# Kernel optimization log

Hardware: AMD Instinct MI355X
Metric: run time of the kernel (lower is better)

The kernel has to match this reference:

```python
import jax, jax.numpy as jnp
import numpy as np

B, C, H, W = 4, 32, 256, 256


def _conv1x1(x, w, b):
    # 1x1 conv == channel-mixing matmul; x: [B,C,H,W], w: [Cout,Cin], b: [Cout]
    return jnp.einsum('oc,bchw->bohw', w, x) + b[None, :, None, None]


def setup_inputs() -> dict:
    key = jax.random.key(0)
    ks = jax.random.split(key, 12)
    inp = {
        'source': jax.random.normal(ks[0], (B, C, H, W), dtype=jnp.float32),
        'target': jax.random.normal(ks[1], (B, C, H, W), dtype=jnp.float32),
        # positional biases: torch.rand -> uniform [0,1)
        'P_v': jax.random.uniform(ks[2], (H, W), dtype=jnp.float32),
        'P_h': jax.random.uniform(ks[3], (W, H), dtype=jnp.float32),
        # 1x1 conv weights (Cout, Cin) + biases, kaiming-ish scale
        'w1v': jax.random.normal(ks[4], (C, C), dtype=jnp.float32) / np.sqrt(C),
        'b1v': jax.random.normal(ks[5], (C,), dtype=jnp.float32) * 0.01,
        'w2v': jax.random.normal(ks[6], (C, C), dtype=jnp.float32) / np.sqrt(C),
        'b2v': jax.random.normal(ks[7], (C,), dtype=jnp.float32) * 0.01,
        'w1h': jax.random.normal(ks[8], (C, C), dtype=jnp.float32) / np.sqrt(C),
        'b1h': jax.random.normal(ks[9], (C,), dtype=jnp.float32) * 0.01,
        'w2h': jax.random.normal(ks[10], (C, C), dtype=jnp.float32) / np.sqrt(C),
        'b2h': jax.random.normal(ks[11], (C,), dtype=jnp.float32) * 0.01,
    }
    return inp


def reference(source, target, P_v, P_h, w1v, b1v, w2v, b2v, w1h, b1h, w2h, b2h):
    # ---- vertical branch (attention along H, independent per column w) ----
    sv = _conv1x1(source + P_v, w1v, b1v)          # [B,C,H,W]
    tv = _conv1x1(target + P_v, w2v, b2v)          # [B,C,H,W]
    # scores_v[b,w,h,g] = sum_c sv[b,c,h,w] * tv[b,c,g,w]   (no softmax in original)
    scores_v = jnp.einsum('bchw,bcgw->bwhg', sv, tv)
    vertical = jnp.einsum('bwhg,bcgw->bchw', scores_v, target)

    # ---- horizontal branch (attention along W, independent per row h) ----
    # original adds P_h (w,h) to x.transpose(2,3); equivalent to adding P_h.T in BCHW
    sh = _conv1x1(source + P_h.T, w1h, b1h)        # [B,C,H,W]
    th = _conv1x1(target + P_h.T, w2h, b2h)        # [B,C,H,W]
    # scores_h[b,h,w,v] = sum_c sh[b,c,h,w] * th[b,c,h,v]
    scores_h = jnp.einsum('bchw,bchv->bhwv', sh, th)
    horizontal = jnp.einsum('bhwv,bchv->bchw', scores_h, target)

    return jnp.concatenate([horizontal, vertical], axis=1)  # [B,2C,H,W]
```

## Files before the change

### kernel.cpp

```cpp
#include <hip/hip_runtime.h>


#define OFF_GH   0
#define OFF_GV   1048576
#define OFF_QH   2097152
#define OFF_TSH  2129920
#define OFF_QV   2162688
#define OFF_TSV  2195456
#define OFF_PH   2228224
#define OFF_PV   2229504

#define FMA4(A, a4, b4) \
  A = fmaf((a4).x,(b4).x, fmaf((a4).y,(b4).y, fmaf((a4).z,(b4).z, fmaf((a4).w,(b4).w,(A)))))

__global__ __launch_bounds__(256) void prep_kernel(
    const float* __restrict__ w1, const float* __restrict__ b1,
    const float* __restrict__ w2, const float* __restrict__ b2,
    float* __restrict__ outp)
{
  __shared__ float lw1[1024], lw2[1024], lb1[32], lb2[32], lr1[32], lr2[32];
  const int t = threadIdx.x;
  for (int k = 0; k < 4; ++k) { lw1[t + 256*k] = w1[t + 256*k]; lw2[t + 256*k] = w2[t + 256*k]; }
  if (t < 32) { lb1[t] = b1[t]; lb2[t] = b2[t]; }
  __syncthreads();
  if (t < 32)      { float s = 0; for (int c = 0; c < 32; ++c) s += lw1[t*32 + c];      lr1[t] = s; }
  else if (t < 64) { int i = t - 32; float s = 0; for (int c = 0; c < 32; ++c) s += lw2[i*32 + c]; lr2[i] = s; }
  __syncthreads();
  for (int k = 0; k < 4; ++k) {
    const int e = t + 256*k, cp = e >> 5, cq = e & 31;
    float s = 0;
    for (int c1 = 0; c1 < 32; ++c1) s += lw1[c1*32 + cp] * lw2[c1*32 + cq];
    outp[e] = s;
  }
  if (t < 32)       { float s = 0; for (int c1 = 0; c1 < 32; ++c1) s += lw1[c1*32 + t]*lr2[c1];        outp[1024 + t] = s; }
  else if (t < 64)  { int i = t-32; float s = 0; for (int c1 = 0; c1 < 32; ++c1) s += lw1[c1*32+i]*lb2[c1]; outp[1056 + i] = s; }
  else if (t < 96)  { int i = t-64; float s = 0; for (int c1 = 0; c1 < 32; ++c1) s += lr1[c1]*lw2[c1*32+i]; outp[1088 + i] = s; }
  else if (t < 128) { int i = t-96; float s = 0; for (int c1 = 0; c1 < 32; ++c1) s += lb1[c1]*lw2[c1*32+i]; outp[1120 + i] = s; }
  else if (t == 128){ float s = 0; for (int i = 0; i < 32; ++i) s += lr1[i]*lr2[i]; outp[1152] = s; }
  else if (t == 129){ float s = 0; for (int i = 0; i < 32; ++i) s += lr1[i]*lb2[i]; outp[1153] = s; }
  else if (t == 130){ float s = 0; for (int i = 0; i < 32; ++i) s += lb1[i]*lr2[i]; outp[1154] = s; }
  else if (t == 131){ float s = 0; for (int i = 0; i < 32; ++i) s += lb1[i]*lb2[i]; outp[1155] = s; }
}

__global__ __launch_bounds__(256) void hgram_kernel(
    const float* __restrict__ T, const float* __restrict__ Ph,
    float* __restrict__ Gws, float* __restrict__ qws, float* __restrict__ tsws)
{
  __shared__ float tile[4][32*68];
  __shared__ float ptile[4][64];
  const int t = threadIdx.x, wave = t >> 6, lane = t & 63;
  const int x = blockIdx.x*4 + wave;
  const int b = x >> 8, r = x & 255;
  const int c1g = lane & 7, c2g = lane >> 3;
  const float* Trow = T + (b*32)*65536 + r*256;
  float* tw = tile[wave];
  float acc[4][4] = {};
  float qa[4] = {}, tsa[4] = {};
  const int l4 = lane >> 4, k16 = lane & 15;

  for (int ch = 0; ch < 4; ++ch) {
    const int k0 = ch*64;
    #pragma unroll
    for (int cc = 0; cc < 8; ++cc) {
      const int c = cc*4 + l4;
      const float4 v = *(const float4*)&Trow[c*65536 + k0 + k16*4];
      *(float4*)&tw[(l4*8 + cc)*68 + k16*4] = v;
    }
    ptile[wave][lane] = Ph[(k0 + lane)*256 + r];
    __syncthreads();
    #pragma unroll
    for (int g4 = 0; g4 < 16; ++g4) {
      float4 av[4], bv[4];
      const float4 p4 = *(const float4*)&ptile[wave][g4*4];
      #pragma unroll
      for (int i = 0; i < 4; ++i) av[i] = *(const float4*)&tw[(8*i + c1g)*68 + g4*4];
      #pragma unroll
      for (int j = 0; j < 4; ++j) bv[j] = *(const float4*)&tw[(8*j + c2g)*68 + g4*4];
      #pragma unroll
      for (int i = 0; i < 4; ++i)
        #pragma unroll
        for (int j = 0; j < 4; ++j) FMA4(acc[i][j], av[i], bv[j]);
      #pragma unroll
      for (int j = 0; j < 4; ++j) {
        FMA4(qa[j], p4, bv[j]);
        tsa[j] += (bv[j].x + bv[j].y) + (bv[j].z + bv[j].w);
      }
    }
    __syncthreads();
  }
  const int gb = x*1024;
  #pragma unroll
  for (int i = 0; i < 4; ++i) {
    float4 o; o.x = acc[i][0]; o.y = acc[i][1]; o.z = acc[i][2]; o.w = acc[i][3];
    *(float4*)&Gws[gb + (4*c1g + i)*32 + 4*c2g] = o;
  }
  if (c1g == 0) {
    float4 q4o; q4o.x = qa[0]; q4o.y = qa[1]; q4o.z = qa[2]; q4o.w = qa[3];
    float4 t4o; t4o.x = tsa[0]; t4o.y = tsa[1]; t4o.z = tsa[2]; t4o.w = tsa[3];
    *(float4*)&qws[x*32 + 4*c2g]  = q4o;
    *(float4*)&tsws[x*32 + 4*c2g] = t4o;
  }
}

__global__ __launch_bounds__(256) void vgram_kernel(
    const float* __restrict__ T, const float* __restrict__ Pv,
    float* __restrict__ Gws, float* __restrict__ qws, float* __restrict__ tsws)
{
  __shared__ float tile[32*292];
  __shared__ float ptile[4][2][36];
  const int blk = blockIdx.x;
  const int xcd = blk & 7, s = blk >> 3;
  const int b = s >> 2, w8l = s & 3;
  const int w0 = (xcd*4 + w8l)*8;
  const int t = threadIdx.x, wave = t >> 6, lane = t & 63;
  const int c1g = lane & 7, c2g = lane >> 3;
  const int lwb = wave*2;
  float acc[2][4][4] = {};
  float qa[2][4] = {}, tsa[2][4] = {};

  for (int chk = 0; chk < 8; ++chk) {
    const int g0 = chk*32;
    __syncthreads();
    #pragma unroll
    for (int p = 0; p < 8; ++p) {
      const int rowid = p*128 + (t >> 1);
      const int c = rowid >> 5, g = rowid & 31, j = t & 1;
      const float4 v = *(const float4*)&T[((b*32 + c)*256 + g0 + g)*256 + w0 + 4*j];
      float* d = &tile[((c&3)*8 + (c>>2))*292 + g];
      d[(4*j+0)*36] = v.x; d[(4*j+1)*36] = v.y; d[(4*j+2)*36] = v.z; d[(4*j+3)*36] = v.w;
    }
    if (lane < 32) ptile[wave][0][lane]    = Pv[(g0 + lane)*256      + w0 + lwb + 0];
    else           ptile[wave][1][lane-32] = Pv[(g0 + lane - 32)*256 + w0 + lwb + 1];
    __syncthreads();
    #pragma unroll
    for (int g4 = 0; g4 < 8; ++g4) {
      #pragma unroll
      for (int lw = 0; lw < 2; ++lw) {
        const int wo = (lwb + lw)*36 + g4*4;
        float4 av[4], bv[4];
        #pragma unroll
        for (int i = 0; i < 4; ++i) av[i] = *(const float4*)&tile[(8*i + c1g)*292 + wo];
        #pragma unroll
        for (int j = 0; j < 4; ++j) bv[j] = *(const float4*)&tile[(8*j + c2g)*292 + wo];
        const float4 p4 = *(const float4*)&ptile[wave][lw][g4*4];
        #pragma unroll
        for (int i = 0; i < 4; ++i)
          #pragma unroll
          for (int j = 0; j < 4; ++j) FMA4(acc[lw][i][j], av[i], bv[j]);
        #pragma unroll
        for (int j = 0; j < 4; ++j) {
          FMA4(qa[lw][j], p4, bv[j]);
          tsa[lw][j] += (bv[j].x + bv[j].y) + (bv[j].z + bv[j].w);
        }
      }
    }
  }
  #pragma unroll
  for (int lw = 0; lw < 2; ++lw) {
    const int w = w0 + lwb + lw;
    const int gb = ((b << 8) + w)*1024;
    #pragma unroll
    for (int i = 0; i < 4; ++i) {
      float4 o; o.x = acc[lw][i][0]; o.y = acc[lw][i][1]; o.z = acc[lw][i][2]; o.w = acc[lw][i][3];
      *(float4*)&Gws[gb + (4*c1g + i)*32 + 4*c2g] = o;
    }
    if (c1g == 0) {
      float4 q4o; q4o.x = qa[lw][0]; q4o.y = qa[lw][1]; q4o.z = qa[lw][2]; q4o.w = qa[lw][3];
      float4 t4o; t4o.x = tsa[lw][0]; t4o.y = tsa[lw][1]; t4o.z = tsa[lw][2]; t4o.w = tsa[lw][3];
      *(float4*)&qws[((b << 8) + w)*32 + 4*c2g]  = q4o;
      *(float4*)&tsws[((b << 8) + w)*32 + 4*c2g] = t4o;
    }
  }
}

__global__ __launch_bounds__(256) void fold_kernel(float* __restrict__ ws)
{
  const int wgid = blockIdx.x*4 + (threadIdx.x >> 6);
  const int lane = threadIdx.x & 63;
  const int n = lane & 31, mg = lane >> 5;
  const bool horiz = (wgid < 1024);
  const int idx = wgid & 1023;
  float* G   = ws + (horiz ? OFF_GH  : OFF_GV)  + idx*1024;
  float* q   = ws + (horiz ? OFF_QH  : OFF_QV)  + idx*32;
  float* tsp = ws + (horiz ? OFF_TSH : OFF_TSV) + idx*32;
  const float* pp = ws + (horiz ? OFF_PH : OFF_PV);
  float facc[16] = {};
  float s1a = 0.f, t1a = 0.f;
  #pragma unroll
  for (int k4 = 0; k4 < 8; ++k4) {
    float g[4];
    #pragma unroll
    for (int e = 0; e < 4; ++e) g[e] = G[(k4*4 + e)*32 + n];
    const float4 u4 = *(const float4*)&pp[1088 + k4*4];
    const float4 v4 = *(const float4*)&pp[1120 + k4*4];
    s1a += u4.x*g[0] + u4.y*g[1] + u4.z*g[2] + u4.w*g[3];
    t1a += v4.x*g[0] + v4.y*g[1] + v4.z*g[2] + v4.w*g[3];
    #pragma unroll
    for (int i = 0; i < 16; ++i) {
      const float4 wc = *(const float4*)&pp[(mg*16 + i)*32 + k4*4];
      facc[i] += wc.x*g[0] + wc.y*g[1] + wc.z*g[2] + wc.w*g[3];
    }
  }
  const float qv = q[n], tv = tsp[n];
  const float al = pp[1152], be = pp[1153], ga = pp[1154], de = pp[1155];
  #pragma unroll
  for (int i = 0; i < 16; ++i) {
    const int m = mg*16 + i;
    G[m*32 + n] = facc[i] + pp[1024 + m]*qv + pp[1056 + m]*tv;
  }
  if (mg == 0) {
    q[n]   = s1a + al*qv + be*tv;
    tsp[n] = t1a + ga*qv + de*tv;
  }
}

__global__ __launch_bounds__(256) void outv_kernel(
    const float* __restrict__ S, const float* __restrict__ Pv,
    const float* __restrict__ Fws, const float* __restrict__ s1ws, const float* __restrict__ t1ws,
    float* __restrict__ out)
{
  __shared__ float tile[32*324];
  __shared__ float oLDS[16*16*33];
  __shared__ float ptile[16*16];
  const int blk = blockIdx.x;
  const int b = blk & 3;
  const int w16 = (blk >> 2) & 15;
  const int hq = blk >> 6;
  const int w0 = w16*16;
  const int t = threadIdx.x, wave = t >> 6, lane = t & 63;
  const int wsel = lane & 3, cg = lane >> 2;
  const int wloc = wave*4 + wsel;
  const int w = w0 + wloc;
  const int fb = ((b << 8) + w);
  float f[2][32];
  #pragma unroll
  for (int c = 0; c < 32; ++c) {
    f[0][c] = Fws[fb*1024 + c*32 + 2*cg + 0];
    f[1][c] = Fws[fb*1024 + c*32 + 2*cg + 1];
  }
  float s1r[2], t1r[2];
  s1r[0] = s1ws[fb*32 + 2*cg];     s1r[1] = s1ws[fb*32 + 2*cg + 1];
  t1r[0] = t1ws[fb*32 + 2*cg];     t1r[1] = t1ws[fb*32 + 2*cg + 1];

  for (int chk = 0; chk < 4; ++chk) {
    const int h0g = hq*64 + chk*16;
    __syncthreads();
    #pragma unroll
    for (int p = 0; p < 8; ++p) {
      const int slot = p*256 + t;
      const int row = slot >> 2, j = slot & 3;
      const int cp = row >> 4, hl = row & 15;
      const float4 v = *(const float4*)&S[((b*32 + cp)*256 + h0g + hl)*256 + w0 + 4*j];
      float* d = &tile[cp*324 + hl];
      d[(4*j+0)*20] = v.x; d[(4*j+1)*20] = v.y; d[(4*j+2)*20] = v.z; d[(4*j+3)*20] = v.w;
    }
    if (t < 64) {
      const int hl = t >> 2, j = t & 3;
      const float4 v = *(const float4*)&Pv[(h0g + hl)*256 + w0 + 4*j];
      ptile[hl*16 + 4*j + 0] = v.x; ptile[hl*16 + 4*j + 1] = v.y;
      ptile[hl*16 + 4*j + 2] = v.z; ptile[hl*16 + 4*j + 3] = v.w;
    }
    __syncthreads();
    float acc[2][16] = {};
    #pragma unroll
    for (int c = 0; c < 32; ++c) {
      const float* rp = &tile[c*324 + wloc*20];
      const float4 s0 = *(const float4*)&rp[0];
      const float4 s1_ = *(const float4*)&rp[4];
      const float4 s2 = *(const float4*)&rp[8];
      const float4 s3 = *(const float4*)&rp[12];
      #pragma unroll
      for (int p = 0; p < 2; ++p) {
        const float fc = f[p][c];
        acc[p][0]  = fmaf(fc, s0.x, acc[p][0]);  acc[p][1]  = fmaf(fc, s0.y, acc[p][1]);
        acc[p][2]  = fmaf(fc, s0.z, acc[p][2]);  acc[p][3]  = fmaf(fc, s0.w, acc[p][3]);
        acc[p][4]  = fmaf(fc, s1_.x, acc[p][4]); acc[p][5]  = fmaf(fc, s1_.y, acc[p][5]);
        acc[p][6]  = fmaf(fc, s1_.z, acc[p][6]); acc[p][7]  = fmaf(fc, s1_.w, acc[p][7]);
        acc[p][8]  = fmaf(fc, s2.x, acc[p][8]);  acc[p][9]  = fmaf(fc, s2.y, acc[p][9]);
        acc[p][10] = fmaf(fc, s2.z, acc[p][10]); acc[p][11] = fmaf(fc, s2.w, acc[p][11]);
        acc[p][12] = fmaf(fc, s3.x, acc[p][12]); acc[p][13] = fmaf(fc, s3.y, acc[p][13]);
        acc[p][14] = fmaf(fc, s3.z, acc[p][14]); acc[p][15] = fmaf(fc, s3.w, acc[p][15]);
      }
    }
    #pragma unroll
    for (int e = 0; e < 16; ++e) {
      const float pv = ptile[e*16 + wloc];
      oLDS[(e*16 + wloc)*33 + 2*cg + 0] = fmaf(pv, s1r[0], acc[0][e] + t1r[0]);
      oLDS[(e*16 + wloc)*33 + 2*cg + 1] = fmaf(pv, s1r[1], acc[1][e] + t1r[1]);
    }
    __syncthreads();
    #pragma unroll
    for (int p = 0; p < 8; ++p) {
      const int row = p*64 + (t >> 2);
      const int c = row & 31, hl = row >> 5;
      const int wq = t & 3;
      float4 o;
      o.x = oLDS[(hl*16 + wq*4 + 0)*33 + c];
      o.y = oLDS[(hl*16 + wq*4 + 1)*33 + c];
      o.z = oLDS[(hl*16 + wq*4 + 2)*33 + c];
      o.w = oLDS[(hl*16 + wq*4 + 3)*33 + c];
      *(float4*)&out[((b*64 + 32 + c)*256 + h0g + hl)*256 + w0 + wq*4] = o;
    }
  }
}

__global__ __launch_bounds__(256) void outh_kernel(
    const float* __restrict__ S, const float* __restrict__ Ph,
    const float* __restrict__ Fws, const float* __restrict__ s1ws, const float* __restrict__ t1ws,
    float* __restrict__ out)
{
  __shared__ float tile[4*1156];
  __shared__ float ptile[4*36];
  const int blk = blockIdx.x;
  const int b = blk & 3;
  const int hq = (blk >> 2) & 63;
  const int whalf = blk >> 8;
  const int h0 = hq*4;
  const int t = threadIdx.x;
  const int wave = t >> 6, lane = t & 63;
  const int cg = lane & 15, wg = lane >> 4;
  const int h = h0 + wave;
  const int base = (b << 8) + h;
  float f[2][32];
  #pragma unroll
  for (int p = 0; p < 2; ++p)
    #pragma unroll
    for (int c = 0; c < 32; ++c)
      f[p][c] = Fws[base*1024 + c*32 + 2*cg + p];
  float s1r[2], t1r[2];
  #pragma unroll
  for (int p = 0; p < 2; ++p) { s1r[p] = s1ws[base*32 + 2*cg + p]; t1r[p] = t1ws[base*32 + 2*cg + p]; }

  for (int wc = 0; wc < 4; ++wc) {
    const int w0 = (whalf*4 + wc) * 32;
    __syncthreads();
    {
      const int wq8 = t & 7, hh = (t >> 3) & 3, cq = t >> 5;
      #pragma unroll
      for (int k = 0; k < 4; ++k) {
        const int c = cq*4 + k;
        const float4 v = *(const float4*)&S[(((b*32 + c)*256) + (h0 + hh))*256 + w0 + wq8*4];
        *(float4*)&tile[hh*1156 + c*36 + wq8*4] = v;
      }
      if (t < 32) {
        #pragma unroll
        for (int hh2 = 0; hh2 < 4; ++hh2)
          ptile[hh2*36 + t] = Ph[(w0 + t)*256 + h0 + hh2];
      }
    }
    __syncthreads();
    float acc[2][8] = {};
    const float* tw = &tile[wave*1156];
    #pragma unroll
    for (int c = 0; c < 32; ++c) {
      const float4 lo = *(const float4*)&tw[c*36 + wg*8];
      const float4 hi = *(const float4*)&tw[c*36 + wg*8 + 4];
      #pragma unroll
      for (int p = 0; p < 2; ++p) {
        acc[p][0] += f[p][c]*lo.x; acc[p][1] += f[p][c]*lo.y;
        acc[p][2] += f[p][c]*lo.z; acc[p][3] += f[p][c]*lo.w;
        acc[p][4] += f[p][c]*hi.x; acc[p][5] += f[p][c]*hi.y;
        acc[p][6] += f[p][c]*hi.z; acc[p][7] += f[p][c]*hi.w;
      }
    }
    #pragma unroll
    for (int p = 0; p < 2; ++p) {
      float4 o1, o2;
      o1.x = acc[p][0] + ptile[wave*36 + wg*8 + 0]*s1r[p] + t1r[p];
      o1.y = acc[p][1] + ptile[wave*36 + wg*8 + 1]*s1r[p] + t1r[p];
      o1.z = acc[p][2] + ptile[wave*36 + wg*8 + 2]*s1r[p] + t1r[p];
      o1.w = acc[p][3] + ptile[wave*36 + wg*8 + 3]*s1r[p] + t1r[p];
      o2.x = acc[p][4] + ptile[wave*36 + wg*8 + 4]*s1r[p] + t1r[p];
      o2.y = acc[p][5] + ptile[wave*36 + wg*8 + 5]*s1r[p] + t1r[p];
      o2.z = acc[p][6] + ptile[wave*36 + wg*8 + 6]*s1r[p] + t1r[p];
      o2.w = acc[p][7] + ptile[wave*36 + wg*8 + 7]*s1r[p] + t1r[p];
      const int ob = (((b*64 + 2*cg + p)*256) + h)*256 + w0 + wg*8;
      *(float4*)&out[ob]     = o1;
      *(float4*)&out[ob + 4] = o2;
    }
  }
}

extern "C" void kernel_launch(void* const* d_in, const int* in_sizes, int n_in,
                              void* d_out, int out_size, void* d_ws, size_t ws_size,
                              hipStream_t stream) {
  const float* src = (const float*)d_in[0];
  const float* tgt = (const float*)d_in[1];
  const float* Pv  = (const float*)d_in[2];
  const float* Ph  = (const float*)d_in[3];
  const float* w1v = (const float*)d_in[4];
  const float* b1v = (const float*)d_in[5];
  const float* w2v = (const float*)d_in[6];
  const float* b2v = (const float*)d_in[7];
  const float* w1h = (const float*)d_in[8];
  const float* b1h = (const float*)d_in[9];
  const float* w2h = (const float*)d_in[10];
  const float* b2h = (const float*)d_in[11];
  float* ws  = (float*)d_ws;
  float* out = (float*)d_out;

  prep_kernel<<<1, 256, 0, stream>>>(w1h, b1h, w2h, b2h, ws + OFF_PH);
  prep_kernel<<<1, 256, 0, stream>>>(w1v, b1v, w2v, b2v, ws + OFF_PV);
  vgram_kernel<<<128, 256, 0, stream>>>(tgt, Pv, ws + OFF_GV, ws + OFF_QV, ws + OFF_TSV);
  hgram_kernel<<<256, 256, 0, stream>>>(tgt, Ph, ws + OFF_GH, ws + OFF_QH, ws + OFF_TSH);
  fold_kernel<<<512, 256, 0, stream>>>(ws);
  outv_kernel<<<256, 256, 0, stream>>>(src, Pv, ws + OFF_GV, ws + OFF_QV, ws + OFF_TSV, out);
  outh_kernel<<<512, 256, 0, stream>>>(src, Ph, ws + OFF_GH, ws + OFF_QH, ws + OFF_TSH, out);
}
```

Measured before the change: 244.0 us.

## Fuse gram and output kernels, split-K gram reduction with atomics

Merges the two prep launches into one grid, and the vertical and horizontal gram kernels into one launch with block-index dispatch. The gram reduction is split along the sequence dimension (4 ways vertical, 2 ways horizontal) and partial sums are combined with float atomics into a workspace zeroed by a memset. The two output kernels are likewise fused into one launch, and the vertical half now covers half as many rows per block so twice as many blocks run. The aim is more blocks in flight and fewer launches, at the cost of atomic traffic, an extra memset and non-deterministic summation order.

```diff
diff --git a/kernel.cpp b/kernel.cpp
--- a/kernel.cpp
+++ b/kernel.cpp
@@ -9,15 +9,22 @@
 #define OFF_TSV  2195456
 #define OFF_PH   2228224
 #define OFF_PV   2229504
+#define ACC_FLOATS 2228224
 
 #define FMA4(A, a4, b4) \
   A = fmaf((a4).x,(b4).x, fmaf((a4).y,(b4).y, fmaf((a4).z,(b4).z, fmaf((a4).w,(b4).w,(A)))))
 
-__global__ __launch_bounds__(256) void prep_kernel(
-    const float* __restrict__ w1, const float* __restrict__ b1,
-    const float* __restrict__ w2, const float* __restrict__ b2,
-    float* __restrict__ outp)
+__global__ __launch_bounds__(256) void prep2_kernel(
+    const float* __restrict__ w1h, const float* __restrict__ b1h,
+    const float* __restrict__ w2h, const float* __restrict__ b2h,
+    const float* __restrict__ w1v, const float* __restrict__ b1v,
+    const float* __restrict__ w2v, const float* __restrict__ b2v,
+    float* __restrict__ ws)
 {
+  const bool V = (blockIdx.x != 0);
+  const float* w1 = V ? w1v : w1h;  const float* b1 = V ? b1v : b1h;
+  const float* w2 = V ? w2v : w2h;  const float* b2 = V ? b2v : b2h;
+  float* outp = ws + (V ? OFF_PV : OFF_PH);
   __shared__ float lw1[1024], lw2[1024], lb1[32], lb2[32], lr1[32], lr2[32];
   const int t = threadIdx.x;
   for (int k = 0; k < 4; ++k) { lw1[t + 256*k] = w1[t + 256*k]; lw2[t + 256*k] = w2[t + 256*k]; }
@@ -42,133 +49,137 @@
   else if (t == 131){ float s = 0; for (int i = 0; i < 32; ++i) s += lb1[i]*lb2[i]; outp[1155] = s; }
 }
 
-__global__ __launch_bounds__(256) void hgram_kernel(
-    const float* __restrict__ T, const float* __restrict__ Ph,
-    float* __restrict__ Gws, float* __restrict__ qws, float* __restrict__ tsws)
+__global__ __launch_bounds__(256) void gram_fused(
+    const float* __restrict__ T, const float* __restrict__ Pv, const float* __restrict__ Ph,
+    float* __restrict__ ws)
 {
-  __shared__ float tile[4][32*68];
-  __shared__ float ptile[4][64];
-  const int t = threadIdx.x, wave = t >> 6, lane = t & 63;
-  const int x = blockIdx.x*4 + wave;
-  const int b = x >> 8, r = x & 255;
-  const int c1g = lane & 7, c2g = lane >> 3;
-  const float* Trow = T + (b*32)*65536 + r*256;
-  float* tw = tile[wave];
-  float acc[4][4] = {};
-  float qa[4] = {}, tsa[4] = {};
-  const int l4 = lane >> 4, k16 = lane & 15;
-
-  for (int ch = 0; ch < 4; ++ch) {
-    const int k0 = ch*64;
-    #pragma unroll
-    for (int cc = 0; cc < 8; ++cc) {
-      const int c = cc*4 + l4;
-      const float4 v = *(const float4*)&Trow[c*65536 + k0 + k16*4];
-      *(float4*)&tw[(l4*8 + cc)*68 + k16*4] = v;
-    }
-    ptile[wave][lane] = Ph[(k0 + lane)*256 + r];
-    __syncthreads();
-    #pragma unroll
-    for (int g4 = 0; g4 < 16; ++g4) {
-      float4 av[4], bv[4];
-      const float4 p4 = *(const float4*)&ptile[wave][g4*4];
-      #pragma unroll
-      for (int i = 0; i < 4; ++i) av[i] = *(const float4*)&tw[(8*i + c1g)*68 + g4*4];
-      #pragma unroll
-      for (int j = 0; j < 4; ++j) bv[j] = *(const float4*)&tw[(8*j + c2g)*68 + g4*4];
-      #pragma unroll
-      for (int i = 0; i < 4; ++i)
-        #pragma unroll
-        for (int j = 0; j < 4; ++j) FMA4(acc[i][j], av[i], bv[j]);
-      #pragma unroll
-      for (int j = 0; j < 4; ++j) {
-        FMA4(qa[j], p4, bv[j]);
-        tsa[j] += (bv[j].x + bv[j].y) + (bv[j].z + bv[j].w);
-      }
-    }
-    __syncthreads();
-  }
-  const int gb = x*1024;
-  #pragma unroll
-  for (int i = 0; i < 4; ++i) {
-    float4 o; o.x = acc[i][0]; o.y = acc[i][1]; o.z = acc[i][2]; o.w = acc[i][3];
-    *(float4*)&Gws[gb + (4*c1g + i)*32 + 4*c2g] = o;
-  }
-  if (c1g == 0) {
-    float4 q4o; q4o.x = qa[0]; q4o.y = qa[1]; q4o.z = qa[2]; q4o.w = qa[3];
-    float4 t4o; t4o.x = tsa[0]; t4o.y = tsa[1]; t4o.z = tsa[2]; t4o.w = tsa[3];
-    *(float4*)&qws[x*32 + 4*c2g]  = q4o;
-    *(float4*)&tsws[x*32 + 4*c2g] = t4o;
-  }
-}
-
-__global__ __launch_bounds__(256) void vgram_kernel(
-    const float* __restrict__ T, const float* __restrict__ Pv,
-    float* __restrict__ Gws, float* __restrict__ qws, float* __restrict__ tsws)
-{
-  __shared__ float tile[32*292];
-  __shared__ float ptile[4][2][36];
+  __shared__ float lds[9632];
   const int blk = blockIdx.x;
-  const int xcd = blk & 7, s = blk >> 3;
-  const int b = s >> 2, w8l = s & 3;
-  const int w0 = (xcd*4 + w8l)*8;
   const int t = threadIdx.x, wave = t >> 6, lane = t & 63;
   const int c1g = lane & 7, c2g = lane >> 3;
-  const int lwb = wave*2;
-  float acc[2][4][4] = {};
-  float qa[2][4] = {}, tsa[2][4] = {};
-
-  for (int chk = 0; chk < 8; ++chk) {
-    const int g0 = chk*32;
-    __syncthreads();
-    #pragma unroll
-    for (int p = 0; p < 8; ++p) {
-      const int rowid = p*128 + (t >> 1);
-      const int c = rowid >> 5, g = rowid & 31, j = t & 1;
-      const float4 v = *(const float4*)&T[((b*32 + c)*256 + g0 + g)*256 + w0 + 4*j];
-      float* d = &tile[((c&3)*8 + (c>>2))*292 + g];
-      d[(4*j+0)*36] = v.x; d[(4*j+1)*36] = v.y; d[(4*j+2)*36] = v.z; d[(4*j+3)*36] = v.w;
-    }
-    if (lane < 32) ptile[wave][0][lane]    = Pv[(g0 + lane)*256      + w0 + lwb + 0];
-    else           ptile[wave][1][lane-32] = Pv[(g0 + lane - 32)*256 + w0 + lwb + 1];
-    __syncthreads();
-    #pragma unroll
-    for (int g4 = 0; g4 < 8; ++g4) {
-      #pragma unroll
-      for (int lw = 0; lw < 2; ++lw) {
-        const int wo = (lwb + lw)*36 + g4*4;
+
+  if (blk < 512) {
+    float* Gws  = ws + OFF_GV;
+    float* qws  = ws + OFF_QV;
+    float* tsws = ws + OFF_TSV;
+    float* tile  = lds;
+    float* ptile = lds + 9344;
+    const int xcd = blk & 7, s = blk >> 3;
+    const int kq = s & 3, b = (s >> 2) & 3, w8l = s >> 4;
+    const int w0 = (xcd*4 + w8l)*8;
+    const int lwb = wave*2;
+    float acc[2][4][4] = {};
+    float qa[2][4] = {}, tsa[2][4] = {};
+    for (int chk = 0; chk < 2; ++chk) {
+      const int g0 = kq*64 + chk*32;
+      __syncthreads();
+      #pragma unroll
+      for (int p = 0; p < 8; ++p) {
+        const int rowid = p*128 + (t >> 1);
+        const int c = rowid >> 5, g = rowid & 31, j = t & 1;
+        const float4 v = *(const float4*)&T[((b*32 + c)*256 + g0 + g)*256 + w0 + 4*j];
+        float* d = &tile[((c&3)*8 + (c>>2))*292 + g];
+        d[(4*j+0)*36] = v.x; d[(4*j+1)*36] = v.y; d[(4*j+2)*36] = v.z; d[(4*j+3)*36] = v.w;
+      }
+      if (lane < 32) ptile[(wave*2+0)*36 + lane]      = Pv[(g0 + lane)*256      + w0 + lwb + 0];
+      else           ptile[(wave*2+1)*36 + lane - 32] = Pv[(g0 + lane - 32)*256 + w0 + lwb + 1];
+      __syncthreads();
+      #pragma unroll
+      for (int g4 = 0; g4 < 8; ++g4) {
+        #pragma unroll
+        for (int lw = 0; lw < 2; ++lw) {
+          const int wo = (lwb + lw)*36 + g4*4;
+          float4 av[4], bv[4];
+          #pragma unroll
+          for (int i = 0; i < 4; ++i) av[i] = *(const float4*)&tile[(8*i + c1g)*292 + wo];
+          #pragma unroll
+          for (int j = 0; j < 4; ++j) bv[j] = *(const float4*)&tile[(8*j + c2g)*292 + wo];
+          const float4 p4 = *(const float4*)&ptile[(wave*2+lw)*36 + g4*4];
+          #pragma unroll
+          for (int i = 0; i < 4; ++i)
+            #pragma unroll
+            for (int j = 0; j < 4; ++j) FMA4(acc[lw][i][j], av[i], bv[j]);
+          #pragma unroll
+          for (int j = 0; j < 4; ++j) {
+            FMA4(qa[lw][j], p4, bv[j]);
+            tsa[lw][j] += (bv[j].x + bv[j].y) + (bv[j].z + bv[j].w);
+          }
+        }
+      }
+    }
+    #pragma unroll
+    for (int lw = 0; lw < 2; ++lw) {
+      const int w = w0 + lwb + lw;
+      const int gb = ((b << 8) + w)*1024;
+      #pragma unroll
+      for (int i = 0; i < 4; ++i)
+        #pragma unroll
+        for (int j = 0; j < 4; ++j)
+          unsafeAtomicAdd(&Gws[gb + (4*c1g + i)*32 + 4*c2g + j], acc[lw][i][j]);
+      if (c1g == 0) {
+        #pragma unroll
+        for (int j = 0; j < 4; ++j) {
+          unsafeAtomicAdd(&qws [((b << 8) + w)*32 + 4*c2g + j], qa[lw][j]);
+          unsafeAtomicAdd(&tsws[((b << 8) + w)*32 + 4*c2g + j], tsa[lw][j]);
+        }
+      }
+    }
+  } else {
+    float* Gws  = ws + OFF_GH;
+    float* qws  = ws + OFF_QH;
+    float* tsws = ws + OFF_TSH;
+    float* tile  = lds + wave*2176;
+    float* ptile = lds + 8704 + wave*64;
+    const int j2 = blk - 512;
+    const int kh = j2 & 1, xblk = j2 >> 1;
+    const int x = xblk*4 + wave;
+    const int b = x >> 8, r = x & 255;
+    const float* Trow = T + (b*32)*65536 + r*256;
+    const int l4 = lane >> 4, k16 = lane & 15;
+    float acc[4][4] = {};
+    float qa[4] = {}, tsa[4] = {};
+    for (int ch = 0; ch < 2; ++ch) {
+      const int k0 = kh*128 + ch*64;
+      __syncthreads();
+      #pragma unroll
+      for (int cc = 0; cc < 8; ++cc) {
+        const int c = cc*4 + l4;
+        const float4 v = *(const float4*)&Trow[c*65536 + k0 + k16*4];
+        *(float4*)&tile[(l4*8 + cc)*68 + k16*4] = v;
+      }
+      ptile[lane] = Ph[(k0 + lane)*256 + r];
+      __syncthreads();
+      #pragma unroll
+      for (int g4 = 0; g4 < 16; ++g4) {
         float4 av[4], bv[4];
-        #pragma unroll
-        for (int i = 0; i < 4; ++i) av[i] = *(const float4*)&tile[(8*i + c1g)*292 + wo];
-        #pragma unroll
-        for (int j = 0; j < 4; ++j) bv[j] = *(const float4*)&tile[(8*j + c2g)*292 + wo];
-        const float4 p4 = *(const float4*)&ptile[wave][lw][g4*4];
+        const float4 p4 = *(const float4*)&ptile[g4*4];
+        #pragma unroll
+        for (int i = 0; i < 4; ++i) av[i] = *(const float4*)&tile[(8*i + c1g)*68 + g4*4];
+        #pragma unroll
+        for (int j = 0; j < 4; ++j) bv[j] = *(const float4*)&tile[(8*j + c2g)*68 + g4*4];
         #pragma unroll
         for (int i = 0; i < 4; ++i)
           #pragma unroll
-          for (int j = 0; j < 4; ++j) FMA4(acc[lw][i][j], av[i], bv[j]);
+          for (int j = 0; j < 4; ++j) FMA4(acc[i][j], av[i], bv[j]);
         #pragma unroll
         for (int j = 0; j < 4; ++j) {
-          FMA4(qa[lw][j], p4, bv[j]);
-          tsa[lw][j] += (bv[j].x + bv[j].y) + (bv[j].z + bv[j].w);
-        }
-      }
-    }
-  }
-  #pragma unroll
-  for (int lw = 0; lw < 2; ++lw) {
-    const int w = w0 + lwb + lw;
-    const int gb = ((b << 8) + w)*1024;
-    #pragma unroll
-    for (int i = 0; i < 4; ++i) {
-      float4 o; o.x = acc[lw][i][0]; o.y = acc[lw][i][1]; o.z = acc[lw][i][2]; o.w = acc[lw][i][3];
-      *(float4*)&Gws[gb + (4*c1g + i)*32 + 4*c2g] = o;
-    }
+          FMA4(qa[j], p4, bv[j]);
+          tsa[j] += (bv[j].x + bv[j].y) + (bv[j].z + bv[j].w);
+        }
+      }
+    }
+    const int gb = x*1024;
+    #pragma unroll
+    for (int i = 0; i < 4; ++i)
+      #pragma unroll
+      for (int j = 0; j < 4; ++j)
+        unsafeAtomicAdd(&Gws[gb + (4*c1g + i)*32 + 4*c2g + j], acc[i][j]);
     if (c1g == 0) {
-      float4 q4o; q4o.x = qa[lw][0]; q4o.y = qa[lw][1]; q4o.z = qa[lw][2]; q4o.w = qa[lw][3];
-      float4 t4o; t4o.x = tsa[lw][0]; t4o.y = tsa[lw][1]; t4o.z = tsa[lw][2]; t4o.w = tsa[lw][3];
-      *(float4*)&qws[((b << 8) + w)*32 + 4*c2g]  = q4o;
-      *(float4*)&tsws[((b << 8) + w)*32 + 4*c2g] = t4o;
+      #pragma unroll
+      for (int j = 0; j < 4; ++j) {
+        unsafeAtomicAdd(&qws [x*32 + 4*c2g + j], qa[j]);
+        unsafeAtomicAdd(&tsws[x*32 + 4*c2g + j], tsa[j]);
+      }
     }
   }
 }
@@ -214,169 +225,173 @@
   }
 }
 
-__global__ __launch_bounds__(256) void outv_kernel(
-    const float* __restrict__ S, const float* __restrict__ Pv,
-    const float* __restrict__ Fws, const float* __restrict__ s1ws, const float* __restrict__ t1ws,
-    float* __restrict__ out)
+__global__ __launch_bounds__(256) void out_fused(
+    const float* __restrict__ S, const float* __restrict__ Pv, const float* __restrict__ Ph,
+    const float* __restrict__ ws, float* __restrict__ out)
 {
-  __shared__ float tile[32*324];
-  __shared__ float oLDS[16*16*33];
-  __shared__ float ptile[16*16];
+  __shared__ float lds[10624];
   const int blk = blockIdx.x;
-  const int b = blk & 3;
-  const int w16 = (blk >> 2) & 15;
-  const int hq = blk >> 6;
-  const int w0 = w16*16;
   const int t = threadIdx.x, wave = t >> 6, lane = t & 63;
-  const int wsel = lane & 3, cg = lane >> 2;
-  const int wloc = wave*4 + wsel;
-  const int w = w0 + wloc;
-  const int fb = ((b << 8) + w);
-  float f[2][32];
-  #pragma unroll
-  for (int c = 0; c < 32; ++c) {
-    f[0][c] = Fws[fb*1024 + c*32 + 2*cg + 0];
-    f[1][c] = Fws[fb*1024 + c*32 + 2*cg + 1];
-  }
-  float s1r[2], t1r[2];
-  s1r[0] = s1ws[fb*32 + 2*cg];     s1r[1] = s1ws[fb*32 + 2*cg + 1];
-  t1r[0] = t1ws[fb*32 + 2*cg];     t1r[1] = t1ws[fb*32 + 2*cg + 1];
-
-  for (int chk = 0; chk < 4; ++chk) {
-    const int h0g = hq*64 + chk*16;
-    __syncthreads();
-    #pragma unroll
-    for (int p = 0; p < 8; ++p) {
-      const int slot = p*256 + t;
-      const int row = slot >> 2, j = slot & 3;
-      const int cp = row >> 4, hl = row & 15;
-      const float4 v = *(const float4*)&S[((b*32 + cp)*256 + h0g + hl)*256 + w0 + 4*j];
-      float* d = &tile[cp*324 + hl];
-      d[(4*j+0)*20] = v.x; d[(4*j+1)*20] = v.y; d[(4*j+2)*20] = v.z; d[(4*j+3)*20] = v.w;
-    }
-    if (t < 64) {
-      const int hl = t >> 2, j = t & 3;
-      const float4 v = *(const float4*)&Pv[(h0g + hl)*256 + w0 + 4*j];
-      ptile[hl*16 + 4*j + 0] = v.x; ptile[hl*16 + 4*j + 1] = v.y;
-      ptile[hl*16 + 4*j + 2] = v.z; ptile[hl*16 + 4*j + 3] = v.w;
-    }
-    __syncthreads();
-    float acc[2][16] = {};
+
+  if (blk < 512) {
+    const float* Fws  = ws + OFF_GV;
+    const float* s1ws = ws + OFF_QV;
+    const float* t1ws = ws + OFF_TSV;
+    float* tile  = lds;
+    float* oLDS  = lds;
+    float* ptile = lds + 10368;
+    const int b = blk & 3;
+    const int w16 = (blk >> 2) & 15;
+    const int h8 = blk >> 6;
+    const int w0 = w16*16;
+    const int wsel = lane & 3, cg = lane >> 2;
+    const int wloc = wave*4 + wsel;
+    const int w = w0 + wloc;
+    const int fb = ((b << 8) + w);
+    float f[2][32];
     #pragma unroll
     for (int c = 0; c < 32; ++c) {
-      const float* rp = &tile[c*324 + wloc*20];
-      const float4 s0 = *(const float4*)&rp[0];
-      const float4 s1_ = *(const float4*)&rp[4];
-      const float4 s2 = *(const float4*)&rp[8];
-      const float4 s3 = *(const float4*)&rp[12];
+      f[0][c] = Fws[fb*1024 + c*32 + 2*cg + 0];
+      f[1][c] = Fws[fb*1024 + c*32 + 2*cg + 1];
+    }
+    float s1r[2], t1r[2];
+    s1r[0] = s1ws[fb*32 + 2*cg];  s1r[1] = s1ws[fb*32 + 2*cg + 1];
+    t1r[0] = t1ws[fb*32 + 2*cg];  t1r[1] = t1ws[fb*32 + 2*cg + 1];
+
+    for (int chk = 0; chk < 2; ++chk) {
+      const int h0g = h8*32 + chk*16;
+      __syncthreads();
+      #pragma unroll
+      for (int p = 0; p < 8; ++p) {
+        const int slot = p*256 + t;
+        const int row = slot >> 2, j = slot & 3;
+        const int cp = row >> 4, hl = row & 15;
+        const float4 v = *(const float4*)&S[((b*32 + cp)*256 + h0g + hl)*256 + w0 + 4*j];
+        float* d = &tile[cp*324 + hl];
+        d[(4*j+0)*20] = v.x; d[(4*j+1)*20] = v.y; d[(4*j+2)*20] = v.z; d[(4*j+3)*20] = v.w;
+      }
+      if (t < 64) {
+        const int hl = t >> 2, j = t & 3;
+        const float4 v = *(const float4*)&Pv[(h0g + hl)*256 + w0 + 4*j];
+        ptile[hl*16 + 4*j + 0] = v.x; ptile[hl*16 + 4*j + 1] = v.y;
+        ptile[hl*16 + 4*j + 2] = v.z; ptile[hl*16 + 4*j + 3] = v.w;
+      }
+      __syncthreads();
+      float acc[2][16] = {};
+      #pragma unroll
+      for (int c = 0; c < 32; ++c) {
+        const float* rp = &tile[c*324 + wloc*20];
+        const float4 s0 = *(const float4*)&rp[0];
+        const float4 s1_ = *(const float4*)&rp[4];
+        const float4 s2 = *(const float4*)&rp[8];
+        const float4 s3 = *(const float4*)&rp[12];
+        #pragma unroll
+        for (int p = 0; p < 2; ++p) {
+          const float fc = f[p][c];
+          acc[p][0]  = fmaf(fc, s0.x, acc[p][0]);  acc[p][1]  = fmaf(fc, s0.y, acc[p][1]);
+          acc[p][2]  = fmaf(fc, s0.z, acc[p][2]);  acc[p][3]  = fmaf(fc, s0.w, acc[p][3]);
+          acc[p][4]  = fmaf(fc, s1_.x, acc[p][4]); acc[p][5]  = fmaf(fc, s1_.y, acc[p][5]);
+          acc[p][6]  = fmaf(fc, s1_.z, acc[p][6]); acc[p][7]  = fmaf(fc, s1_.w, acc[p][7]);
+          acc[p][8]  = fmaf(fc, s2.x, acc[p][8]);  acc[p][9]  = fmaf(fc, s2.y, acc[p][9]);
+          acc[p][10] = fmaf(fc, s2.z, acc[p][10]); acc[p][11] = fmaf(fc, s2.w, acc[p][11]);
+          acc[p][12] = fmaf(fc, s3.x, acc[p][12]); acc[p][13] = fmaf(fc, s3.y, acc[p][13]);
+          acc[p][14] = fmaf(fc, s3.z, acc[p][14]); acc[p][15] = fmaf(fc, s3.w, acc[p][15]);
+        }
+      }
+      float pcol[16];
+      #pragma unroll
+      for (int e = 0; e < 16; ++e) pcol[e] = ptile[e*16 + wloc];
+      __syncthreads();
+      #pragma unroll
+      for (int e = 0; e < 16; ++e) {
+        oLDS[(e*16 + wloc)*33 + 2*cg + 0] = fmaf(pcol[e], s1r[0], acc[0][e] + t1r[0]);
+        oLDS[(e*16 + wloc)*33 + 2*cg + 1] = fmaf(pcol[e], s1r[1], acc[1][e] + t1r[1]);
+      }
+      __syncthreads();
+      #pragma unroll
+      for (int p = 0; p < 8; ++p) {
+        const int row = p*64 + (t >> 2);
+        const int c = row & 31, hl = row >> 5;
+        const int wq = t & 3;
+        float4 o;
+        o.x = oLDS[(hl*16 + wq*4 + 0)*33 + c];
+        o.y = oLDS[(hl*16 + wq*4 + 1)*33 + c];
+        o.z = oLDS[(hl*16 + wq*4 + 2)*33 + c];
+        o.w = oLDS[(hl*16 + wq*4 + 3)*33 + c];
+        *(float4*)&out[((b*64 + 32 + c)*256 + h0g + hl)*256 + w0 + wq*4] = o;
+      }
+    }
+  } else {
+    const float* Fws  = ws + OFF_GH;
+    const float* s1ws = ws + OFF_QH;
+    const float* t1ws = ws + OFF_TSH;
+    float* tile  = lds;
+    float* ptile = lds + 4624;
+    const int blk2 = blk - 512;
+    const int b = blk2 & 3;
+    const int hq = (blk2 >> 2) & 63;
+    const int whalf = blk2 >> 8;
+    const int h0 = hq*4;
+    const int cg = lane & 15, wg = lane >> 4;
+    const int h = h0 + wave;
+    const int base = (b << 8) + h;
+    float f[2][32];
+    #pragma unroll
+    for (int p = 0; p < 2; ++p)
+      #pragma unroll
+      for (int c = 0; c < 32; ++c)
+        f[p][c] = Fws[base*1024 + c*32 + 2*cg + p];
+    float s1r[2], t1r[2];
+    #pragma unroll
+    for (int p = 0; p < 2; ++p) { s1r[p] = s1ws[base*32 + 2*cg + p]; t1r[p] = t1ws[base*32 + 2*cg + p]; }
+
+    for (int wc = 0; wc < 4; ++wc) {
+      const int w0 = (whalf*4 + wc) * 32;
+      __syncthreads();
+      {
+        const int wq8 = t & 7, hh = (t >> 3) & 3, cq = t >> 5;
+        #pragma unroll
+        for (int k = 0; k < 4; ++k) {
+          const int c = cq*4 + k;
+          const float4 v = *(const float4*)&S[(((b*32 + c)*256) + (h0 + hh))*256 + w0 + wq8*4];
+          *(float4*)&tile[hh*1156 + c*36 + wq8*4] = v;
+        }
+        if (t < 32) {
+          #pragma unroll
+          for (int hh2 = 0; hh2 < 4; ++hh2)
+            ptile[hh2*36 + t] = Ph[(w0 + t)*256 + h0 + hh2];
+        }
+      }
+      __syncthreads();
+      float acc[2][8] = {};
+      const float* tw = &tile[wave*1156];
+      #pragma unroll
+      for (int c = 0; c < 32; ++c) {
+        const float4 lo = *(const float4*)&tw[c*36 + wg*8];
+        const float4 hi = *(const float4*)&tw[c*36 + wg*8 + 4];
+        #pragma unroll
+        for (int p = 0; p < 2; ++p) {
+          acc[p][0] += f[p][c]*lo.x; acc[p][1] += f[p][c]*lo.y;
+          acc[p][2] += f[p][c]*lo.z; acc[p][3] += f[p][c]*lo.w;
+          acc[p][4] += f[p][c]*hi.x; acc[p][5] += f[p][c]*hi.y;
+          acc[p][6] += f[p][c]*hi.z; acc[p][7] += f[p][c]*hi.w;
+        }
+      }
       #pragma unroll
       for (int p = 0; p < 2; ++p) {
-        const float fc = f[p][c];
-        acc[p][0]  = fmaf(fc, s0.x, acc[p][0]);  acc[p][1]  = fmaf(fc, s0.y, acc[p][1]);
-        acc[p][2]  = fmaf(fc, s0.z, acc[p][2]);  acc[p][3]  = fmaf(fc, s0.w, acc[p][3]);
-        acc[p][4]  = fmaf(fc, s1_.x, acc[p][4]); acc[p][5]  = fmaf(fc, s1_.y, acc[p][5]);
-        acc[p][6]  = fmaf(fc, s1_.z, acc[p][6]); acc[p][7]  = fmaf(fc, s1_.w, acc[p][7]);
-        acc[p][8]  = fmaf(fc, s2.x, acc[p][8]);  acc[p][9]  = fmaf(fc, s2.y, acc[p][9]);
-        acc[p][10] = fmaf(fc, s2.z, acc[p][10]); acc[p][11] = fmaf(fc, s2.w, acc[p][11]);
-        acc[p][12] = fmaf(fc, s3.x, acc[p][12]); acc[p][13] = fmaf(fc, s3.y, acc[p][13]);
-        acc[p][14] = fmaf(fc, s3.z, acc[p][14]); acc[p][15] = fmaf(fc, s3.w, acc[p][15]);
-      }
-    }
-    #pragma unroll
-    for (int e = 0; e < 16; ++e) {
-      const float pv = ptile[e*16 + wloc];
-      oLDS[(e*16 + wloc)*33 + 2*cg + 0] = fmaf(pv, s1r[0], acc[0][e] + t1r[0]);
-      oLDS[(e*16 + wloc)*33 + 2*cg + 1] = fmaf(pv, s1r[1], acc[1][e] + t1r[1]);
-    }
-    __syncthreads();
-    #pragma unroll
-    for (int p = 0; p < 8; ++p) {
-      const int row = p*64 + (t >> 2);
-      const int c = row & 31, hl = row >> 5;
-      const int wq = t & 3;
-      float4 o;
-      o.x = oLDS[(hl*16 + wq*4 + 0)*33 + c];
-      o.y = oLDS[(hl*16 + wq*4 + 1)*33 + c];
-      o.z = oLDS[(hl*16 + wq*4 + 2)*33 + c];
-      o.w = oLDS[(hl*16 + wq*4 + 3)*33 + c];
-      *(float4*)&out[((b*64 + 32 + c)*256 + h0g + hl)*256 + w0 + wq*4] = o;
-    }
-  }
-}
-
-__global__ __launch_bounds__(256) void outh_kernel(
-    const float* __restrict__ S, const float* __restrict__ Ph,
-    const float* __restrict__ Fws, const float* __restrict__ s1ws, const float* __restrict__ t1ws,
-    float* __restrict__ out)
-{
-  __shared__ float tile[4*1156];
-  __shared__ float ptile[4*36];
-  const int blk = blockIdx.x;
-  const int b = blk & 3;
-  const int hq = (blk >> 2) & 63;
-  const int whalf = blk >> 8;
-  const int h0 = hq*4;
-  const int t = threadIdx.x;
-  const int wave = t >> 6, lane = t & 63;
-  const int cg = lane & 15, wg = lane >> 4;
-  const int h = h0 + wave;
-  const int base = (b << 8) + h;
-  float f[2][32];
-  #pragma unroll
-  for (int p = 0; p < 2; ++p)
-    #pragma unroll
-    for (int c = 0; c < 32; ++c)
-      f[p][c] = Fws[base*1024 + c*32 + 2*cg + p];
-  float s1r[2], t1r[2];
-  #pragma unroll
-  for (int p = 0; p < 2; ++p) { s1r[p] = s1ws[base*32 + 2*cg + p]; t1r[p] = t1ws[base*32 + 2*cg + p]; }
-
-  for (int wc = 0; wc < 4; ++wc) {
-    const int w0 = (whalf*4 + wc) * 32;
-    __syncthreads();
-    {
-      const int wq8 = t & 7, hh = (t >> 3) & 3, cq = t >> 5;
-      #pragma unroll
-      for (int k = 0; k < 4; ++k) {
-        const int c = cq*4 + k;
-        const float4 v = *(const float4*)&S[(((b*32 + c)*256) + (h0 + hh))*256 + w0 + wq8*4];
-        *(float4*)&tile[hh*1156 + c*36 + wq8*4] = v;
-      }
-      if (t < 32) {
-        #pragma unroll
-        for (int hh2 = 0; hh2 < 4; ++hh2)
-          ptile[hh2*36 + t] = Ph[(w0 + t)*256 + h0 + hh2];
-      }
-    }
-    __syncthreads();
-    float acc[2][8] = {};
-    const float* tw = &tile[wave*1156];
-    #pragma unroll
-    for (int c = 0; c < 32; ++c) {
-      const float4 lo = *(const float4*)&tw[c*36 + wg*8];
-      const float4 hi = *(const float4*)&tw[c*36 + wg*8 + 4];
-      #pragma unroll
-      for (int p = 0; p < 2; ++p) {
-        acc[p][0] += f[p][c]*lo.x; acc[p][1] += f[p][c]*lo.y;
-        acc[p][2] += f[p][c]*lo.z; acc[p][3] += f[p][c]*lo.w;
-        acc[p][4] += f[p][c]*hi.x; acc[p][5] += f[p][c]*hi.y;
-        acc[p][6] += f[p][c]*hi.z; acc[p][7] += f[p][c]*hi.w;
-      }
-    }
-    #pragma unroll
-    for (int p = 0; p < 2; ++p) {
-      float4 o1, o2;
-      o1.x = acc[p][0] + ptile[wave*36 + wg*8 + 0]*s1r[p] + t1r[p];
-      o1.y = acc[p][1] + ptile[wave*36 + wg*8 + 1]*s1r[p] + t1r[p];
-      o1.z = acc[p][2] + ptile[wave*36 + wg*8 + 2]*s1r[p] + t1r[p];
-      o1.w = acc[p][3] + ptile[wave*36 + wg*8 + 3]*s1r[p] + t1r[p];
-      o2.x = acc[p][4] + ptile[wave*36 + wg*8 + 4]*s1r[p] + t1r[p];
-      o2.y = acc[p][5] + ptile[wave*36 + wg*8 + 5]*s1r[p] + t1r[p];
-      o2.z = acc[p][6] + ptile[wave*36 + wg*8 + 6]*s1r[p] + t1r[p];
-      o2.w = acc[p][7] + ptile[wave*36 + wg*8 + 7]*s1r[p] + t1r[p];
-      const int ob = (((b*64 + 2*cg + p)*256) + h)*256 + w0 + wg*8;
-      *(float4*)&out[ob]     = o1;
-      *(float4*)&out[ob + 4] = o2;
+        float4 o1, o2;
+        o1.x = acc[p][0] + ptile[wave*36 + wg*8 + 0]*s1r[p] + t1r[p];
+        o1.y = acc[p][1] + ptile[wave*36 + wg*8 + 1]*s1r[p] + t1r[p];
+        o1.z = acc[p][2] + ptile[wave*36 + wg*8 + 2]*s1r[p] + t1r[p];
+        o1.w = acc[p][3] + ptile[wave*36 + wg*8 + 3]*s1r[p] + t1r[p];
+        o2.x = acc[p][4] + ptile[wave*36 + wg*8 + 4]*s1r[p] + t1r[p];
+        o2.y = acc[p][5] + ptile[wave*36 + wg*8 + 5]*s1r[p] + t1r[p];
+        o2.z = acc[p][6] + ptile[wave*36 + wg*8 + 6]*s1r[p] + t1r[p];
+        o2.w = acc[p][7] + ptile[wave*36 + wg*8 + 7]*s1r[p] + t1r[p];
+        const int ob = (((b*64 + 2*cg + p)*256) + h)*256 + w0 + wg*8;
+        *(float4*)&out[ob]     = o1;
+        *(float4*)&out[ob + 4] = o2;
+      }
     }
   }
 }
@@ -399,11 +414,9 @@
   float* ws  = (float*)d_ws;
   float* out = (float*)d_out;
 
-  prep_kernel<<<1, 256, 0, stream>>>(w1h, b1h, w2h, b2h, ws + OFF_PH);
-  prep_kernel<<<1, 256, 0, stream>>>(w1v, b1v, w2v, b2v, ws + OFF_PV);
-  vgram_kernel<<<128, 256, 0, stream>>>(tgt, Pv, ws + OFF_GV, ws + OFF_QV, ws + OFF_TSV);
-  hgram_kernel<<<256, 256, 0, stream>>>(tgt, Ph, ws + OFF_GH, ws + OFF_QH, ws + OFF_TSH);
+  hipMemsetAsync(d_ws, 0, (size_t)ACC_FLOATS*4, stream);
+  prep2_kernel<<<2, 256, 0, stream>>>(w1h, b1h, w2h, b2h, w1v, b1v, w2v, b2v, ws);
+  gram_fused<<<1024, 256, 0, stream>>>(tgt, Pv, Ph, ws);
   fold_kernel<<<512, 256, 0, stream>>>(ws);
-  outv_kernel<<<256, 256, 0, stream>>>(src, Pv, ws + OFF_GV, ws + OFF_QV, ws + OFF_TSV, out);
-  outh_kernel<<<512, 256, 0, stream>>>(src, Ph, ws + OFF_GH, ws + OFF_QH, ws + OFF_TSH, out);
+  out_fused<<<1024, 256, 0, stream>>>(src, Pv, Ph, ws, out);
 }
```

Result: slower. 299.5 us (+22.8%).
